# Kernel optimization log

Hardware: AMD Instinct MI355X
Metric: run time of the kernel (lower is better)

Reference implementation:

```python
import jax, jax.numpy as jnp
import numpy as np

N_LAYERS = 512
Z_INI = 0.0
DEL_Z = 0.9 / 512.0
MU = 1.0
BATCH = 131072


def setup_inputs() -> dict:
    key = jax.random.key(0)
    k1, k2, k3, k4 = jax.random.split(key, 4)
    Re_s = 0.1 * jax.random.normal(k1, (BATCH,), dtype=jnp.float32)
    Im_s = 0.1 * jax.random.normal(k2, (BATCH,), dtype=jnp.float32)
    # omega kept away from 0 (appears in a denominator)
    omega = jax.random.uniform(k3, (BATCH,), dtype=jnp.float32, minval=0.5, maxval=1.5)
    PiT = jnp.ones((1,), dtype=jnp.float32)
    # Bs[j] is Linear(1,1,bias=False)(ones) == its scalar weight; keep near 1 for stability
    B = 1.0 + 0.02 * jax.random.normal(k4, (N_LAYERS + 1,), dtype=jnp.float32)
    return {"Re_s": Re_s, "Im_s": Im_s, "omega": omega, "PiT": PiT, "B": B}


def reference(Re_s, Im_s, omega, PiT, B):
    # forward_1: Euler integration, strict sequential dependence -> lax.scan
    zs = Z_INI + DEL_Z * jnp.arange(N_LAYERS, dtype=jnp.float32)
    B1s = B[:-1]  # Bs[j]
    B2s = B[1:]   # Bs[j+1]
    mu2 = MU * MU

    def step(carry, x):
        Re, Im = carry
        b1, b2, z = x
        inv1 = 1.0 / (PiT * (1.0 - z))          # 1/(PiT (1-z))
        inv2 = inv1 / (1.0 - z)                  # 1/(PiT (1-z)^2)
        g = 1.0 - b2 / b1
        # NOTE: torch updates Re first; Im update uses the NEW Re
        Re_n = Re + g * (Re + inv1) + DEL_Z * (
            2.0 * omega * Im * Re + 2.0 * omega * Im * inv1 - inv2
        )
        Im_n = Im + g * Im + DEL_Z * (
            -omega * inv2 / PiT
            - 2.0 * omega * inv1 * Re_n
            + omega * Im * Im
            - omega * Re_n * Re_n
            + omega / (b1 * b1)
            - z * z * mu2 / (b1 * omega)
        )
        return (Re_n, Im_n), None

    (Re_f, Im_f), _ = jax.lax.scan(step, (Re_s, Im_s), (B1s, B2s, zs))
    return (Re_f, Im_f)
```

## Files before the change

### kernel.cpp

```cpp
#include <hip/hip_runtime.h>

#define N_LAYERS 512
#define DEL_Z (0.9f / 512.0f)

__global__ __launch_bounds__(256) void metric_scan_kernel(
    const float* __restrict__ Re_s, const float* __restrict__ Im_s,
    const float* __restrict__ omega, const float* __restrict__ PiT_p,
    const float* __restrict__ B, float* __restrict__ out, int n)
{
    __shared__ float4 cA[N_LAYERS];
    __shared__ float  cB[N_LAYERS];

    const float PiT = PiT_p[0];
    for (int l = threadIdx.x; l < N_LAYERS; l += 256) {
        const float z    = DEL_Z * (float)l;
        const float b1   = B[l];
        const float b2   = B[l + 1];
        const float omz  = 1.0f - z;
        const float inv1 = 1.0f / (PiT * omz);
        const float inv2 = inv1 / omz;
        const float g    = 1.0f - b2 / b1;
        const float c0   = 1.0f + g;
        const float c1   = g * inv1 - DEL_Z * inv2;
        const float c3   = inv1 * inv1 - inv2 / PiT + 1.0f / (b1 * b1);
        const float c4   = DEL_Z * z * z / b1;
        cA[l] = make_float4(c0, c1, inv1, c3);
        cB[l] = c4;
    }
    __syncthreads();

    const int i = blockIdx.x * 256 + threadIdx.x;
    float Re = Re_s[i];
    float Im = Im_s[i];
    const float om    = omega[i];
    const float dzom  = DEL_Z * om;
    const float dz2om = 2.0f * dzom;
    const float iom   = 1.0f / om;

    #pragma unroll 8
    for (int l = 0; l < N_LAYERS; ++l) {
        const float4 c  = cA[l];
        const float  c4 = cB[l];
        const float  t  = Re + c.z;
        const float  a  = fmaf(c.x, Re, c.y);
        const float  Rn = fmaf(dz2om * Im, t, a);
        const float  u  = Rn + c.z;
        float s = fmaf(Im, Im, c.w);
        s = fmaf(-u, u, s);
        const float b = fmaf(c.x, Im, -(c4 * iom));
        Im = fmaf(dzom, s, b);
        Re = Rn;
    }

    out[i]     = Re;
    out[n + i] = Im;
}

extern "C" void kernel_launch(void* const* d_in, const int* in_sizes, int n_in,
                              void* d_out, int out_size, void* d_ws, size_t ws_size,
                              hipStream_t stream)
{
    const float* Re_s  = (const float*)d_in[0];
    const float* Im_s  = (const float*)d_in[1];
    const float* omega = (const float*)d_in[2];
    const float* PiT   = (const float*)d_in[3];
    const float* B     = (const float*)d_in[4];
    float* out = (float*)d_out;
    const int n = in_sizes[0];
    metric_scan_kernel<<<n / 256, 256, 0, stream>>>(Re_s, Im_s, omega, PiT, B, out, n);
}
```

Measured before the change: 21.57 us.

## Precompute layer coefficients in separate kernel and read them as uniform global loads

Moves the per-layer coefficient setup into a small kernel that writes a structure-of-arrays table to workspace, so the scan kernel no longer recomputes the table in every block or waits on a block barrier. The scan loop reads coefficients from global memory with wave-uniform indices, which the compiler can turn into scalar loads instead of LDS reads. It also reshapes the Im update to use omega^-2 times a coefficient. The cost is a second kernel launch and a dependence on workspace memory.

Measured after the change: 32.58 us. 1.51x slower.

```diff
diff --git a/kernel.cpp b/kernel.cpp
--- a/kernel.cpp
+++ b/kernel.cpp
@@ -3,31 +3,37 @@
 #define N_LAYERS 512
 #define DEL_Z (0.9f / 512.0f)
 
+__global__ __launch_bounds__(256) void metric_setup_kernel(
+    const float* __restrict__ PiT_p, const float* __restrict__ B,
+    float* __restrict__ C)
+{
+    const int l = blockIdx.x * 256 + threadIdx.x;
+    if (l >= N_LAYERS) return;
+    const float PiT  = PiT_p[0];
+    const float z    = DEL_Z * (float)l;
+    const float b1   = B[l];
+    const float b2   = B[l + 1];
+    const float omz  = 1.0f - z;
+    const float inv1 = 1.0f / (PiT * omz);
+    const float inv2 = inv1 / omz;
+    const float g    = 1.0f - b2 / b1;
+    C[0 * N_LAYERS + l] = 1.0f + g;
+    C[1 * N_LAYERS + l] = g * inv1 - DEL_Z * inv2;
+    C[2 * N_LAYERS + l] = inv1;
+    C[3 * N_LAYERS + l] = inv1 * inv1 - inv2 / PiT + 1.0f / (b1 * b1);
+    C[4 * N_LAYERS + l] = z * z / b1;
+}
+
 __global__ __launch_bounds__(256) void metric_scan_kernel(
     const float* __restrict__ Re_s, const float* __restrict__ Im_s,
-    const float* __restrict__ omega, const float* __restrict__ PiT_p,
-    const float* __restrict__ B, float* __restrict__ out, int n)
+    const float* __restrict__ omega, const float* __restrict__ C,
+    float* __restrict__ out, int n)
 {
-    __shared__ float4 cA[N_LAYERS];
-    __shared__ float  cB[N_LAYERS];
-
-    const float PiT = PiT_p[0];
-    for (int l = threadIdx.x; l < N_LAYERS; l += 256) {
-        const float z    = DEL_Z * (float)l;
-        const float b1   = B[l];
-        const float b2   = B[l + 1];
-        const float omz  = 1.0f - z;
-        const float inv1 = 1.0f / (PiT * omz);
-        const float inv2 = inv1 / omz;
-        const float g    = 1.0f - b2 / b1;
-        const float c0   = 1.0f + g;
-        const float c1   = g * inv1 - DEL_Z * inv2;
-        const float c3   = inv1 * inv1 - inv2 / PiT + 1.0f / (b1 * b1);
-        const float c4   = DEL_Z * z * z / b1;
-        cA[l] = make_float4(c0, c1, inv1, c3);
-        cB[l] = c4;
-    }
-    __syncthreads();
+    const float* __restrict__ C0 = C + 0 * N_LAYERS;
+    const float* __restrict__ C1 = C + 1 * N_LAYERS;
+    const float* __restrict__ CI = C + 2 * N_LAYERS;
+    const float* __restrict__ C3 = C + 3 * N_LAYERS;
+    const float* __restrict__ C4 = C + 4 * N_LAYERS;
 
     const int i = blockIdx.x * 256 + threadIdx.x;
     float Re = Re_s[i];
@@ -36,18 +42,24 @@
     const float dzom  = DEL_Z * om;
     const float dz2om = 2.0f * dzom;
     const float iom   = 1.0f / om;
+    const float iom2  = iom * iom;
 
     #pragma unroll 8
     for (int l = 0; l < N_LAYERS; ++l) {
-        const float4 c  = cA[l];
-        const float  c4 = cB[l];
-        const float  t  = Re + c.z;
-        const float  a  = fmaf(c.x, Re, c.y);
-        const float  Rn = fmaf(dz2om * Im, t, a);
-        const float  u  = Rn + c.z;
-        float s = fmaf(Im, Im, c.w);
+        const float c0 = C0[l];
+        const float c1 = C1[l];
+        const float i1 = CI[l];
+        const float c3 = C3[l];
+        const float c4 = C4[l];
+        const float t  = Re + i1;
+        const float a  = fmaf(c0, Re, c1);
+        const float m  = dz2om * Im;
+        const float Rn = fmaf(m, t, a);
+        const float u  = Rn + i1;
+        float s = fmaf(Im, Im, c3);
+        s = fmaf(-c4, iom2, s);
+        const float b = c0 * Im;
         s = fmaf(-u, u, s);
-        const float b = fmaf(c.x, Im, -(c4 * iom));
         Im = fmaf(dzom, s, b);
         Re = Rn;
     }
@@ -66,6 +78,9 @@
     const float* PiT   = (const float*)d_in[3];
     const float* B     = (const float*)d_in[4];
     float* out = (float*)d_out;
+    float* C   = (float*)d_ws;
     const int n = in_sizes[0];
-    metric_scan_kernel<<<n / 256, 256, 0, stream>>>(Re_s, Im_s, omega, PiT, B, out, n);
+
+    metric_setup_kernel<<<2, 256, 0, stream>>>(PiT, B, C);
+    metric_scan_kernel<<<n / 256, 256, 0, stream>>>(Re_s, Im_s, omega, C, out, n);
 }
```

## Process two elements per thread with SoA-transposed constants and double-buffered LDS loads

Applied to the files above, without the earlier changes.

Each thread now integrates two batch elements, so every per-layer constant loaded from shared memory is reused twice and the two independent recurrences can interleave to hide dependency latency. Constants are laid out in groups of four layers with one float4 per coefficient, and the next group is prefetched into registers while the current group is computed. The grid is halved, which lowers occupancy and raises register use per thread.

Result: slower. 29.29 us (+35.8%).

```diff
diff --git a/kernel.cpp b/kernel.cpp
--- a/kernel.cpp
+++ b/kernel.cpp
@@ -2,16 +2,50 @@
 
 #define N_LAYERS 512
 #define DEL_Z (0.9f / 512.0f)
+#define NGROUP (N_LAYERS / 4)
+
+
+#define STEP1(RE, IM, DZOM, DZ2OM, NIOM, C0, C1, I1, C3, C4P)   \
+    {                                                           \
+        const float t  = (RE) + (I1);                           \
+        const float a  = fmaf((C0), (RE), (C1));                \
+        const float m  = (DZ2OM) * (IM);                        \
+        const float Rn = fmaf(m, t, a);                         \
+        const float u  = Rn + (I1);                             \
+        float s = fmaf((IM), (IM), (C3));                       \
+        s = fmaf(-u, u, s);                                     \
+        const float q  = (C4P) * (NIOM);                        \
+        const float b  = fmaf((C0), (IM), q);                   \
+        (IM) = fmaf((DZOM), s, b);                              \
+        (RE) = Rn;                                              \
+    }
+
+#define STEP2(C0, C1, I1, C3, C4P)                              \
+    STEP1(Re0, Im0, dzom0, dz2om0, niom0, C0, C1, I1, C3, C4P)  \
+    STEP1(Re1, Im1, dzom1, dz2om1, niom1, C0, C1, I1, C3, C4P)
+
+#define GROUP4(A0, A1, A2, A3, A4)                              \
+    STEP2((A0).x, (A1).x, (A2).x, (A3).x, (A4).x)               \
+    STEP2((A0).y, (A1).y, (A2).y, (A3).y, (A4).y)               \
+    STEP2((A0).z, (A1).z, (A2).z, (A3).z, (A4).z)               \
+    STEP2((A0).w, (A1).w, (A2).w, (A3).w, (A4).w)
+
+#define LOADG(A0, A1, A2, A3, A4, G)                            \
+    {                                                           \
+        const float4* cp = cg[(G)];                             \
+        (A0) = cp[0]; (A1) = cp[1]; (A2) = cp[2];               \
+        (A3) = cp[3]; (A4) = cp[4];                             \
+    }
 
 __global__ __launch_bounds__(256) void metric_scan_kernel(
     const float* __restrict__ Re_s, const float* __restrict__ Im_s,
     const float* __restrict__ omega, const float* __restrict__ PiT_p,
     const float* __restrict__ B, float* __restrict__ out, int n)
 {
-    __shared__ float4 cA[N_LAYERS];
-    __shared__ float  cB[N_LAYERS];
+    __shared__ float4 cg[NGROUP][5];
 
     const float PiT = PiT_p[0];
+    float* cbase = (float*)cg;
     for (int l = threadIdx.x; l < N_LAYERS; l += 256) {
         const float z    = DEL_Z * (float)l;
         const float b1   = B[l];
@@ -20,40 +54,41 @@
         const float inv1 = 1.0f / (PiT * omz);
         const float inv2 = inv1 / omz;
         const float g    = 1.0f - b2 / b1;
-        const float c0   = 1.0f + g;
-        const float c1   = g * inv1 - DEL_Z * inv2;
-        const float c3   = inv1 * inv1 - inv2 / PiT + 1.0f / (b1 * b1);
-        const float c4   = DEL_Z * z * z / b1;
-        cA[l] = make_float4(c0, c1, inv1, c3);
-        cB[l] = c4;
+        float* p = cbase + (l >> 2) * 20 + (l & 3);
+        p[0]  = 1.0f + g;
+        p[4]  = g * inv1 - DEL_Z * inv2;
+        p[8]  = inv1;
+        p[12] = inv1 * inv1 - inv2 / PiT + 1.0f / (b1 * b1);
+        p[16] = DEL_Z * z * z / b1;
     }
     __syncthreads();
 
-    const int i = blockIdx.x * 256 + threadIdx.x;
-    float Re = Re_s[i];
-    float Im = Im_s[i];
-    const float om    = omega[i];
-    const float dzom  = DEL_Z * om;
-    const float dz2om = 2.0f * dzom;
-    const float iom   = 1.0f / om;
+    const int half = n >> 1;
+    const int e0 = blockIdx.x * 256 + threadIdx.x;
+    const int e1 = e0 + half;
 
-    #pragma unroll 8
-    for (int l = 0; l < N_LAYERS; ++l) {
-        const float4 c  = cA[l];
-        const float  c4 = cB[l];
-        const float  t  = Re + c.z;
-        const float  a  = fmaf(c.x, Re, c.y);
-        const float  Rn = fmaf(dz2om * Im, t, a);
-        const float  u  = Rn + c.z;
-        float s = fmaf(Im, Im, c.w);
-        s = fmaf(-u, u, s);
-        const float b = fmaf(c.x, Im, -(c4 * iom));
-        Im = fmaf(dzom, s, b);
-        Re = Rn;
+    float Re0 = Re_s[e0], Im0 = Im_s[e0];
+    float Re1 = Re_s[e1], Im1 = Im_s[e1];
+    const float om0 = omega[e0], om1 = omega[e1];
+    const float dzom0 = DEL_Z * om0, dz2om0 = 2.0f * dzom0, niom0 = -1.0f / om0;
+    const float dzom1 = DEL_Z * om1, dz2om1 = 2.0f * dzom1, niom1 = -1.0f / om1;
+
+    float4 Pa0, Pa1, Pa2, Pa3, Pa4;
+    float4 Pb0, Pb1, Pb2, Pb3, Pb4;
+    LOADG(Pa0, Pa1, Pa2, Pa3, Pa4, 0);
+
+    for (int g = 0; g < NGROUP; g += 2) {
+        LOADG(Pb0, Pb1, Pb2, Pb3, Pb4, g + 1);
+        GROUP4(Pa0, Pa1, Pa2, Pa3, Pa4);
+        const int gn = (g + 2 < NGROUP) ? g + 2 : NGROUP - 1;
+        LOADG(Pa0, Pa1, Pa2, Pa3, Pa4, gn);
+        GROUP4(Pb0, Pb1, Pb2, Pb3, Pb4);
     }
 
-    out[i]     = Re;
-    out[n + i] = Im;
+    out[e0]     = Re0;
+    out[n + e0] = Im0;
+    out[e1]     = Re1;
+    out[n + e1] = Im1;
 }
 
 extern "C" void kernel_launch(void* const* d_in, const int* in_sizes, int n_in,
@@ -67,5 +102,6 @@
     const float* B     = (const float*)d_in[4];
     float* out = (float*)d_out;
     const int n = in_sizes[0];
-    metric_scan_kernel<<<n / 256, 256, 0, stream>>>(Re_s, Im_s, omega, PiT, B, out, n);
+    const int nthreads = n / 2;
+    metric_scan_kernel<<<nthreads / 256, 256, 0, stream>>>(Re_s, Im_s, omega, PiT, B, out, n);
 }
```

## Carry shifted Re variable and broadcast per-layer constants via readlane

Applied to the files above, without the earlier changes.

Reformulates the recurrence to carry t = Re + inv1, so each layer needs fewer adds and only the difference of consecutive inv1 terms. Per-layer constants are laid out so each wave loads one float4 per lane per 32-layer chunk, and the values are broadcast with readlane as scalar operands instead of per-layer LDS loads. The next chunk is prefetched while the current one is processed. This cuts LDS traffic and VALU ops inside the serial dependency chain. The cost is a fully unrolled 32-step inner loop and a slightly different float rounding order.

After: 30.06 us. +39.4%, slower.

```diff
diff --git a/kernel.cpp b/kernel.cpp
--- a/kernel.cpp
+++ b/kernel.cpp
@@ -2,57 +2,78 @@
 
 #define N_LAYERS 512
 #define DEL_Z (0.9f / 512.0f)
+#define NMACRO (N_LAYERS / 32)
+
+
+__device__ __forceinline__ float rl(float v, int lane) {
+    return __int_as_float(__builtin_amdgcn_readlane(__float_as_int(v), lane));
+}
 
 __global__ __launch_bounds__(256) void metric_scan_kernel(
     const float* __restrict__ Re_s, const float* __restrict__ Im_s,
     const float* __restrict__ omega, const float* __restrict__ PiT_p,
     const float* __restrict__ B, float* __restrict__ out, int n)
 {
-    __shared__ float4 cA[N_LAYERS];
-    __shared__ float  cB[N_LAYERS];
+    __shared__ float cls[N_LAYERS * 8];
 
     const float PiT = PiT_p[0];
     for (int l = threadIdx.x; l < N_LAYERS; l += 256) {
-        const float z    = DEL_Z * (float)l;
-        const float b1   = B[l];
-        const float b2   = B[l + 1];
-        const float omz  = 1.0f - z;
-        const float inv1 = 1.0f / (PiT * omz);
-        const float inv2 = inv1 / omz;
-        const float g    = 1.0f - b2 / b1;
-        const float c0   = 1.0f + g;
-        const float c1   = g * inv1 - DEL_Z * inv2;
-        const float c3   = inv1 * inv1 - inv2 / PiT + 1.0f / (b1 * b1);
-        const float c4   = DEL_Z * z * z / b1;
-        cA[l] = make_float4(c0, c1, inv1, c3);
-        cB[l] = c4;
+        const float z     = DEL_Z * (float)l;
+        const float b1    = B[l];
+        const float b2    = B[l + 1];
+        const float omz   = 1.0f - z;
+        const float inv1  = 1.0f / (PiT * omz);
+        const float inv2  = inv1 / omz;
+        const float zn    = DEL_Z * (float)(l + 1);
+        const float inv1n = 1.0f / (PiT * (1.0f - zn));
+        const float g     = 1.0f - b2 / b1;
+        float* p = cls + ((l >> 5) * 256 + (l & 31) * 8);
+        p[0] = 1.0f + g;
+        p[1] = -DEL_Z * inv2;
+        p[2] = inv1n - inv1;
+        p[3] = inv1 * inv1 - inv2 / PiT + 1.0f / (b1 * b1);
+        p[4] = DEL_Z * z * z / b1;
     }
     __syncthreads();
 
     const int i = blockIdx.x * 256 + threadIdx.x;
-    float Re = Re_s[i];
     float Im = Im_s[i];
     const float om    = omega[i];
     const float dzom  = DEL_Z * om;
     const float dz2om = 2.0f * dzom;
-    const float iom   = 1.0f / om;
+    const float niom  = -1.0f / om;
+    float t = Re_s[i] + 1.0f / PiT;
 
-    #pragma unroll 8
-    for (int l = 0; l < N_LAYERS; ++l) {
-        const float4 c  = cA[l];
-        const float  c4 = cB[l];
-        const float  t  = Re + c.z;
-        const float  a  = fmaf(c.x, Re, c.y);
-        const float  Rn = fmaf(dz2om * Im, t, a);
-        const float  u  = Rn + c.z;
-        float s = fmaf(Im, Im, c.w);
-        s = fmaf(-u, u, s);
-        const float b = fmaf(c.x, Im, -(c4 * iom));
-        Im = fmaf(dzom, s, b);
-        Re = Rn;
+    const float4* cf4 = (const float4*)cls;
+    const int lane = threadIdx.x & 63;
+
+    float4 va = cf4[lane];
+    for (int G = 0; G < NMACRO; ++G) {
+        const int Gn = (G + 1 < NMACRO) ? G + 1 : NMACRO - 1;
+        float4 vb = cf4[Gn * 64 + lane];
+        #pragma unroll
+        for (int m = 0; m < 32; ++m) {
+            const float c0  = rl(va.x, 2 * m);
+            const float d1  = rl(va.y, 2 * m);
+            const float dl  = rl(va.z, 2 * m);
+            const float c3  = rl(va.w, 2 * m);
+            const float c4p = rl(va.x, 2 * m + 1);
+            const float e = fmaf(dz2om, Im, c0);
+            const float u = fmaf(e, t, d1);
+            float s = fmaf(Im, Im, c3);
+            const float q = c4p * niom;
+            const float b = fmaf(c0, Im, q);
+            s = fmaf(-u, u, s);
+            t = u + dl;
+            Im = fmaf(dzom, s, b);
+        }
+        va = vb;
     }
 
-    out[i]     = Re;
+    const float zend = DEL_Z * 512.0f;
+    const float Re_f = t - 1.0f / (PiT * (1.0f - zend));
+
+    out[i]     = Re_f;
     out[n + i] = Im;
 }
 
```
